# Performance work log

Hardware: AMD Instinct MI355X
Metric: run time of the kernel (lower is better)

The kernel has to match this reference:

```python
import jax, jax.numpy as jnp
import numpy as np

K = 50          # nearest neighbours
IMG = 224       # output mask resolution
SIGMA = 4.0     # gaussian blur sigma -> kernel size 2*round(4*sigma)+1 = 33


def _gaussian_blur(m, sigma=SIGMA):
    # separable gaussian blur with reflect padding (matches cv2 BORDER_REFLECT_101)
    ks = 2 * int(round(4 * sigma)) + 1
    r = ks // 2
    x = jnp.arange(ks, dtype=m.dtype) - r
    k1 = jnp.exp(-(x * x) / (2.0 * sigma * sigma))
    k1 = k1 / jnp.sum(k1)
    p = jnp.pad(m, ((0, 0), (r, r), (r, r), (0, 0)), mode='reflect')
    dn = ('NHWC', 'HWIO', 'NHWC')
    p = jax.lax.conv_general_dilated(p, k1.reshape(ks, 1, 1, 1), (1, 1), 'VALID', dimension_numbers=dn)
    p = jax.lax.conv_general_dilated(p, k1.reshape(1, ks, 1, 1), (1, 1), 'VALID', dimension_numbers=dn)
    return p


def setup_inputs() -> dict:
    key = jax.random.key(0)
    ks = jax.random.split(key, 6)
    B, N = 4, 500
    return {
        'x0': jax.random.normal(ks[0], (B, 28, 28, 512), dtype=jnp.float32),
        'x1': jax.random.normal(ks[1], (B, 14, 14, 1024), dtype=jnp.float32),
        'x2': jax.random.normal(ks[2], (B, 1, 1, 2048), dtype=jnp.float32),
        'f0': jax.random.normal(ks[3], (N, 28, 28, 512), dtype=jnp.float32),
        'f1': jax.random.normal(ks[4], (N, 14, 14, 1024), dtype=jnp.float32),
        'f2': jax.random.normal(ks[5], (N, 1, 1, 2048), dtype=jnp.float32),
    }


def reference(x0, x1, x2, f0, f1, f2):
    B = x2.shape[0]
    N = f2.shape[0]
    q = x2.reshape(B, -1)          # [B, D] pooled query embeddings
    bank = f2.reshape(N, -1)       # [N, D] memory bank embeddings
    # pairwise euclidean distance matrix [B, N]
    d2 = (jnp.sum(q * q, axis=1)[:, None]
          + jnp.sum(bank * bank, axis=1)[None, :]
          - 2.0 * (q @ bank.T))
    dist = jnp.sqrt(jnp.maximum(d2, 0.0))
    # k smallest distances + their indices (== ascending sort truncated at k)
    neg_vals, idx = jax.lax.top_k(-dist, K)   # [B, K]
    score = jnp.mean(-neg_vals, axis=-1, keepdims=True)  # [B, 1]
    masks = []
    for f, x in ((f0, x0), (f1, x1)):
        g = f[idx]                                    # gather: [B, K, H, W, C]
        d = jnp.sqrt(jnp.sum((g - x[:, None]) ** 2, axis=-1))  # [B, K, H, W]
        m = jnp.min(d, axis=1)                        # [B, H, W]
        m = jax.image.resize(m[..., None], (B, IMG, IMG, 1), method='bilinear')
        masks.append(m)
    mask = (masks[0] + masks[1]) / 2.0
    mask = _gaussian_blur(mask)
    return score, mask
```

## Files before the change

### kernel.cpp

```cpp
#include <hip/hip_runtime.h>
#include <math.h>

#define B_ 4
#define N_ 500
#define K_ 50
#define D_ 2048
#define IMG_ 224

__global__ void dist_kernel(const float* __restrict__ x2, const float* __restrict__ f2,
                            float* __restrict__ dist) {
  const int n = blockIdx.x, b = blockIdx.y;
  const float* q = x2 + (size_t)b * D_;
  const float* r = f2 + (size_t)n * D_;
  float s = 0.f;
  for (int c = threadIdx.x; c < D_; c += 256) {
    float d = q[c] - r[c];
    s += d * d;
  }
  for (int o = 32; o; o >>= 1) s += __shfl_down(s, o);
  __shared__ float part[4];
  const int lane = threadIdx.x & 63, wv = threadIdx.x >> 6;
  if (lane == 0) part[wv] = s;
  __syncthreads();
  if (threadIdx.x == 0)
    dist[b * N_ + n] = sqrtf(part[0] + part[1] + part[2] + part[3]);
}

__global__ void topk_kernel(const float* __restrict__ dist, int* __restrict__ idx,
                            float* __restrict__ score) {
  const int b = blockIdx.x;
  const int lane = threadIdx.x;
  float v[8];
  int id[8];
  int cnt = 0;
  for (int n = lane; n < N_; n += 64) { v[cnt] = dist[b * N_ + n]; id[cnt] = n; cnt++; }
  for (int c = cnt; c < 8; c++) { v[c] = INFINITY; id[c] = -1; }
  float ssum = 0.f;
  for (int k = 0; k < K_; k++) {
    float bestv = v[0];
    int besti = 0;
#pragma unroll
    for (int c = 1; c < 8; c++)
      if (v[c] < bestv) { bestv = v[c]; besti = c; }
    unsigned long long key =
        ((unsigned long long)__float_as_uint(bestv) << 32) | (unsigned)lane;
    for (int o = 32; o; o >>= 1) {
      unsigned long long other = __shfl_xor(key, o);
      if (other < key) key = other;
    }
    const int wl = (int)(key & 63u);
    const float wvmin = __uint_as_float((unsigned)(key >> 32));
    if (lane == wl) {
      idx[b * K_ + k] = id[besti];
      v[besti] = INFINITY;
    }
    ssum += wvmin;
  }
  if (lane == 0) score[b] = ssum / (float)K_;
}

template <int C, int H>
__global__ __launch_bounds__(256) void mindist_kernel(
    const float* __restrict__ f, const float* __restrict__ x,
    const int* __restrict__ idx, float* __restrict__ m) {
  const int p = blockIdx.x;
  const int b = p / (H * H);
  const int hw = p % (H * H);
  const int lane = threadIdx.x & 63;
  const int wv = threadIdx.x >> 6;
  constexpr int V = C / 256;
  const float4* xrow = (const float4*)(x + ((size_t)b * H * H + hw) * C);
  float4 xv[V];
#pragma unroll
  for (int i = 0; i < V; i++) xv[i] = xrow[lane + i * 64];
  float best = INFINITY;
  for (int k = wv; k < K_; k += 4) {
    const int n = idx[b * K_ + k];
    const float4* frow = (const float4*)(f + ((size_t)n * H * H + hw) * C);
    float s = 0.f;
#pragma unroll
    for (int i = 0; i < V; i++) {
      float4 fv = frow[lane + i * 64];
      float d0 = fv.x - xv[i].x, d1 = fv.y - xv[i].y;
      float d2 = fv.z - xv[i].z, d3 = fv.w - xv[i].w;
      s += d0 * d0 + d1 * d1 + d2 * d2 + d3 * d3;
    }
    for (int o = 32; o; o >>= 1) s += __shfl_down(s, o);
    if (lane == 0) best = fminf(best, s);
  }
  __shared__ float red[4];
  if (lane == 0) red[wv] = best;
  __syncthreads();
  if (threadIdx.x == 0)
    m[p] = sqrtf(fminf(fminf(red[0], red[1]), fminf(red[2], red[3])));
}

__global__ void gk_kernel(float* __restrict__ gk) {
  __shared__ float w[33];
  const int t = threadIdx.x;
  if (t < 33) {
    float xx = (float)t - 16.f;
    w[t] = expf(-(xx * xx) / 32.f);
  }
  __syncthreads();
  if (t == 0) {
    float s = 0.f;
    for (int i = 0; i < 33; i++) s += w[i];
    for (int i = 0; i < 33; i++) gk[i] = w[i] / s;
  }
}

__device__ inline float bilerp(const float* __restrict__ m, int H, int i, int j) {
  const float scale = (float)H / (float)IMG_;
  float ty = fminf(fmaxf(((float)i + 0.5f) * scale - 0.5f, 0.f), (float)(H - 1));
  float tx = fminf(fmaxf(((float)j + 0.5f) * scale - 0.5f, 0.f), (float)(H - 1));
  const int y0 = (int)ty, x0 = (int)tx;
  const int y1 = y0 + 1 < H ? y0 + 1 : H - 1;
  const int x1 = x0 + 1 < H ? x0 + 1 : H - 1;
  const float wy = ty - (float)y0, wx = tx - (float)x0;
  const float a = m[y0 * H + x0] * (1.f - wx) + m[y0 * H + x1] * wx;
  const float c = m[y1 * H + x0] * (1.f - wx) + m[y1 * H + x1] * wx;
  return a * (1.f - wy) + c * wy;
}

__global__ void upsample_kernel(const float* __restrict__ m0, const float* __restrict__ m1,
                                float* __restrict__ up) {
  const int t = blockIdx.x * 256 + threadIdx.x;
  if (t >= B_ * IMG_ * IMG_) return;
  const int b = t / (IMG_ * IMG_);
  const int r = t % (IMG_ * IMG_);
  const int i = r / IMG_, j = r % IMG_;
  const float a0 = bilerp(m0 + b * 28 * 28, 28, i, j);
  const float a1 = bilerp(m1 + b * 14 * 14, 14, i, j);
  up[t] = 0.5f * (a0 + a1);
}

__device__ inline int reflect101(int t) {
  t = t < 0 ? -t : t;
  t = t > IMG_ - 1 ? 2 * (IMG_ - 1) - t : t;
  return t;
}

__global__ void blurH_kernel(const float* __restrict__ up, float* __restrict__ tmp,
                             const float* __restrict__ gk) {
  const int t = blockIdx.x * 256 + threadIdx.x;
  if (t >= B_ * IMG_ * IMG_) return;
  const int b = t / (IMG_ * IMG_);
  const int r = t % (IMG_ * IMG_);
  const int i = r / IMG_, j = r % IMG_;
  float s = 0.f;
#pragma unroll
  for (int o = 0; o < 33; o++) {
    const int y = reflect101(i - 16 + o);
    s += gk[o] * up[(b * IMG_ + y) * IMG_ + j];
  }
  tmp[t] = s;
}

__global__ void blurW_kernel(const float* __restrict__ tmp, float* __restrict__ outm,
                             const float* __restrict__ gk) {
  const int t = blockIdx.x * 256 + threadIdx.x;
  if (t >= B_ * IMG_ * IMG_) return;
  const int b = t / (IMG_ * IMG_);
  const int r = t % (IMG_ * IMG_);
  const int i = r / IMG_, j = r % IMG_;
  float s = 0.f;
#pragma unroll
  for (int o = 0; o < 33; o++) {
    const int xx = reflect101(j - 16 + o);
    s += gk[o] * tmp[(b * IMG_ + i) * IMG_ + xx];
  }
  outm[t] = s;
}

extern "C" void kernel_launch(void* const* d_in, const int* in_sizes, int n_in,
                              void* d_out, int out_size, void* d_ws, size_t ws_size,
                              hipStream_t stream) {
  const float* x0 = (const float*)d_in[0];
  const float* x1 = (const float*)d_in[1];
  const float* x2 = (const float*)d_in[2];
  const float* f0 = (const float*)d_in[3];
  const float* f1 = (const float*)d_in[4];
  const float* f2 = (const float*)d_in[5];
  float* out = (float*)d_out;

  float* ws = (float*)d_ws;
  float* dist = ws;
  int* idxb = (int*)(ws + 2000);
  float* m0 = ws + 2200;
  float* m1 = ws + 5336;
  float* gk = ws + 6120;
  float* up = ws + 6160;
  float* tmp = ws + 206864;

  dist_kernel<<<dim3(N_, B_), 256, 0, stream>>>(x2, f2, dist);
  topk_kernel<<<B_, 64, 0, stream>>>(dist, idxb, out);
  gk_kernel<<<1, 64, 0, stream>>>(gk);
  mindist_kernel<512, 28><<<B_ * 28 * 28, 256, 0, stream>>>(f0, x0, idxb, m0);
  mindist_kernel<1024, 14><<<B_ * 14 * 14, 256, 0, stream>>>(f1, x1, idxb, m1);
  const int npix = B_ * IMG_ * IMG_;
  upsample_kernel<<<npix / 256, 256, 0, stream>>>(m0, m1, up);
  blurH_kernel<<<npix / 256, 256, 0, stream>>>(up, tmp, gk);
  blurW_kernel<<<npix / 256, 256, 0, stream>>>(tmp, out + B_, gk);
}
```

Baseline: 1.126 ms.

## Fuse mindist launches, prefetch gathered rows, and fuse upsample+blur into tiled kernel

Merges the two per-level min-distance kernels into a single 512-thread launch. That launch caches the top-k indices in shared memory and prefetches the next gathered feature row while the current one is reduced. The upsample, vertical blur and horizontal blur passes become one shared-memory tiled kernel that computes the Gaussian weights in-block, which removes the separate weight kernel and the global intermediates. The reference distance kernel is also vectorised with float4 loads. The costs are more launches and global round-trips avoided, against redundant halo computation per tile and higher register pressure from double-buffered rows.

Measured after the change: 1.117 ms. Within noise of the previous version (-0.8%).

```diff
diff --git a/kernel.cpp b/kernel.cpp
--- a/kernel.cpp
+++ b/kernel.cpp
@@ -10,12 +10,16 @@
 __global__ void dist_kernel(const float* __restrict__ x2, const float* __restrict__ f2,
                             float* __restrict__ dist) {
   const int n = blockIdx.x, b = blockIdx.y;
-  const float* q = x2 + (size_t)b * D_;
-  const float* r = f2 + (size_t)n * D_;
+  const float4* q = (const float4*)(x2 + (size_t)b * D_);
+  const float4* r = (const float4*)(f2 + (size_t)n * D_);
   float s = 0.f;
-  for (int c = threadIdx.x; c < D_; c += 256) {
-    float d = q[c] - r[c];
-    s += d * d;
+#pragma unroll
+  for (int c = 0; c < 2; c++) {
+    const float4 qa = q[threadIdx.x + c * 256];
+    const float4 ra = r[threadIdx.x + c * 256];
+    const float d0 = qa.x - ra.x, d1 = qa.y - ra.y;
+    const float d2 = qa.z - ra.z, d3 = qa.w - ra.w;
+    s += d0 * d0 + d1 * d1 + d2 * d2 + d3 * d3;
   }
   for (int o = 32; o; o >>= 1) s += __shfl_down(s, o);
   __shared__ float part[4];
@@ -60,12 +64,11 @@
 }
 
 template <int C, int H>
-__global__ __launch_bounds__(256) void mindist_kernel(
-    const float* __restrict__ f, const float* __restrict__ x,
-    const int* __restrict__ idx, float* __restrict__ m) {
-  const int p = blockIdx.x;
+__device__ void mindist_body(const float* __restrict__ f, const float* __restrict__ x,
+                             const int* idx_s, float* red, float* __restrict__ m,
+                             const int p) {
   const int b = p / (H * H);
-  const int hw = p % (H * H);
+  const int hw = p - b * (H * H);
   const int lane = threadIdx.x & 63;
   const int wv = threadIdx.x >> 6;
   constexpr int V = C / 256;
@@ -74,40 +77,62 @@
 #pragma unroll
   for (int i = 0; i < V; i++) xv[i] = xrow[lane + i * 64];
   float best = INFINITY;
-  for (int k = wv; k < K_; k += 4) {
-    const int n = idx[b * K_ + k];
-    const float4* frow = (const float4*)(f + ((size_t)n * H * H + hw) * C);
-    float s = 0.f;
-#pragma unroll
-    for (int i = 0; i < V; i++) {
-      float4 fv = frow[lane + i * 64];
-      float d0 = fv.x - xv[i].x, d1 = fv.y - xv[i].y;
-      float d2 = fv.z - xv[i].z, d3 = fv.w - xv[i].w;
-      s += d0 * d0 + d1 * d1 + d2 * d2 + d3 * d3;
+  int k = wv;
+  {
+    const float4* frow = (const float4*)(f + ((size_t)idx_s[k] * H * H + hw) * C);
+    float4 fv[V];
+#pragma unroll
+    for (int i = 0; i < V; i++) fv[i] = frow[lane + i * 64];
+    while (true) {
+      const int k2 = k + 8;
+      float4 gv[V];
+      if (k2 < K_) {
+        const float4* grow = (const float4*)(f + ((size_t)idx_s[k2] * H * H + hw) * C);
+#pragma unroll
+        for (int i = 0; i < V; i++) gv[i] = grow[lane + i * 64];
+      }
+      float s = 0.f;
+#pragma unroll
+      for (int i = 0; i < V; i++) {
+        const float d0 = fv[i].x - xv[i].x, d1 = fv[i].y - xv[i].y;
+        const float d2 = fv[i].z - xv[i].z, d3 = fv[i].w - xv[i].w;
+        s += d0 * d0 + d1 * d1 + d2 * d2 + d3 * d3;
+      }
+#pragma unroll
+      for (int o = 32; o; o >>= 1) s += __shfl_down(s, o);
+      best = fminf(best, s);
+      if (k2 >= K_) break;
+#pragma unroll
+      for (int i = 0; i < V; i++) fv[i] = gv[i];
+      k = k2;
     }
-    for (int o = 32; o; o >>= 1) s += __shfl_down(s, o);
-    if (lane == 0) best = fminf(best, s);
-  }
-  __shared__ float red[4];
+  }
   if (lane == 0) red[wv] = best;
   __syncthreads();
-  if (threadIdx.x == 0)
-    m[p] = sqrtf(fminf(fminf(red[0], red[1]), fminf(red[2], red[3])));
-}
-
-__global__ void gk_kernel(float* __restrict__ gk) {
-  __shared__ float w[33];
-  const int t = threadIdx.x;
-  if (t < 33) {
-    float xx = (float)t - 16.f;
-    w[t] = expf(-(xx * xx) / 32.f);
-  }
-  __syncthreads();
-  if (t == 0) {
-    float s = 0.f;
-    for (int i = 0; i < 33; i++) s += w[i];
-    for (int i = 0; i < 33; i++) gk[i] = w[i] / s;
-  }
+  if (threadIdx.x == 0) {
+    float r = red[0];
+#pragma unroll
+    for (int w = 1; w < 8; w++) r = fminf(r, red[w]);
+    m[p] = sqrtf(r);
+  }
+}
+
+__global__ __launch_bounds__(512) void mindist_all(
+    const float* __restrict__ f0, const float* __restrict__ x0,
+    const float* __restrict__ f1, const float* __restrict__ x1,
+    const int* __restrict__ idx, float* __restrict__ m0, float* __restrict__ m1) {
+  __shared__ int idx_s[K_];
+  __shared__ float red[8];
+  const int bid = blockIdx.x;
+  const int isF1 = bid >= B_ * 28 * 28;
+  const int p = isF1 ? bid - B_ * 28 * 28 : bid;
+  const int b = isF1 ? p / (14 * 14) : p / (28 * 28);
+  if (threadIdx.x < K_) idx_s[threadIdx.x] = idx[b * K_ + threadIdx.x];
+  __syncthreads();
+  if (!isF1)
+    mindist_body<512, 28>(f0, x0, idx_s, red, m0, p);
+  else
+    mindist_body<1024, 14>(f1, x1, idx_s, red, m1, p);
 }
 
 __device__ inline float bilerp(const float* __restrict__ m, int H, int i, int j) {
@@ -123,54 +148,63 @@
   return a * (1.f - wy) + c * wy;
 }
 
-__global__ void upsample_kernel(const float* __restrict__ m0, const float* __restrict__ m1,
-                                float* __restrict__ up) {
-  const int t = blockIdx.x * 256 + threadIdx.x;
-  if (t >= B_ * IMG_ * IMG_) return;
-  const int b = t / (IMG_ * IMG_);
-  const int r = t % (IMG_ * IMG_);
-  const int i = r / IMG_, j = r % IMG_;
-  const float a0 = bilerp(m0 + b * 28 * 28, 28, i, j);
-  const float a1 = bilerp(m1 + b * 14 * 14, 14, i, j);
-  up[t] = 0.5f * (a0 + a1);
-}
-
 __device__ inline int reflect101(int t) {
   t = t < 0 ? -t : t;
   t = t > IMG_ - 1 ? 2 * (IMG_ - 1) - t : t;
   return t;
 }
 
-__global__ void blurH_kernel(const float* __restrict__ up, float* __restrict__ tmp,
-                             const float* __restrict__ gk) {
-  const int t = blockIdx.x * 256 + threadIdx.x;
-  if (t >= B_ * IMG_ * IMG_) return;
-  const int b = t / (IMG_ * IMG_);
-  const int r = t % (IMG_ * IMG_);
-  const int i = r / IMG_, j = r % IMG_;
-  float s = 0.f;
-#pragma unroll
-  for (int o = 0; o < 33; o++) {
-    const int y = reflect101(i - 16 + o);
-    s += gk[o] * up[(b * IMG_ + y) * IMG_ + j];
-  }
-  tmp[t] = s;
-}
-
-__global__ void blurW_kernel(const float* __restrict__ tmp, float* __restrict__ outm,
-                             const float* __restrict__ gk) {
-  const int t = blockIdx.x * 256 + threadIdx.x;
-  if (t >= B_ * IMG_ * IMG_) return;
-  const int b = t / (IMG_ * IMG_);
-  const int r = t % (IMG_ * IMG_);
-  const int i = r / IMG_, j = r % IMG_;
-  float s = 0.f;
-#pragma unroll
-  for (int o = 0; o < 33; o++) {
-    const int xx = reflect101(j - 16 + o);
-    s += gk[o] * tmp[(b * IMG_ + i) * IMG_ + xx];
-  }
-  outm[t] = s;
+__global__ __launch_bounds__(256) void mask_kernel(const float* __restrict__ m0,
+                                                   const float* __restrict__ m1,
+                                                   float* __restrict__ outm) {
+  __shared__ float gk_s[33];
+  __shared__ float inv2;
+  __shared__ float up_s[64][64];
+  __shared__ float tmp_s[32][64];
+  const int tid = threadIdx.x;
+  const int tx0 = blockIdx.x * 32, ty0 = blockIdx.y * 32, b = blockIdx.z;
+
+  if (tid < 33) {
+    const float xx = (float)tid - 16.f;
+    gk_s[tid] = expf(-(xx * xx) / 32.f);
+  }
+  __syncthreads();
+  if (tid == 0) {
+    float s = 0.f;
+#pragma unroll
+    for (int i = 0; i < 33; i++) s += gk_s[i];
+    inv2 = 1.f / (s * s);
+  }
+
+  const float* mb0 = m0 + b * 28 * 28;
+  const float* mb1 = m1 + b * 14 * 14;
+#pragma unroll
+  for (int e = tid; e < 64 * 64; e += 256) {
+    const int yy = e >> 6, xx = e & 63;
+    const int iy = reflect101(ty0 + yy - 16);
+    const int ix = reflect101(tx0 + xx - 16);
+    const float a0 = bilerp(mb0, 28, iy, ix);
+    const float a1 = bilerp(mb1, 14, iy, ix);
+    up_s[yy][xx] = 0.5f * (a0 + a1);
+  }
+  __syncthreads();
+#pragma unroll
+  for (int e = tid; e < 32 * 64; e += 256) {
+    const int y = e >> 6, x = e & 63;
+    float s = 0.f;
+#pragma unroll
+    for (int o = 0; o < 33; o++) s += gk_s[o] * up_s[y + o][x];
+    tmp_s[y][x] = s;
+  }
+  __syncthreads();
+#pragma unroll
+  for (int e = tid; e < 32 * 32; e += 256) {
+    const int y = e >> 5, x = e & 31;
+    float s = 0.f;
+#pragma unroll
+    for (int o = 0; o < 33; o++) s += gk_s[o] * tmp_s[y][x + o];
+    outm[((size_t)b * IMG_ + (ty0 + y)) * IMG_ + (tx0 + x)] = s * inv2;
+  }
 }
 
 extern "C" void kernel_launch(void* const* d_in, const int* in_sizes, int n_in,
@@ -189,17 +223,9 @@
   int* idxb = (int*)(ws + 2000);
   float* m0 = ws + 2200;
   float* m1 = ws + 5336;
-  float* gk = ws + 6120;
-  float* up = ws + 6160;
-  float* tmp = ws + 206864;
 
   dist_kernel<<<dim3(N_, B_), 256, 0, stream>>>(x2, f2, dist);
   topk_kernel<<<B_, 64, 0, stream>>>(dist, idxb, out);
-  gk_kernel<<<1, 64, 0, stream>>>(gk);
-  mindist_kernel<512, 28><<<B_ * 28 * 28, 256, 0, stream>>>(f0, x0, idxb, m0);
-  mindist_kernel<1024, 14><<<B_ * 14 * 14, 256, 0, stream>>>(f1, x1, idxb, m1);
-  const int npix = B_ * IMG_ * IMG_;
-  upsample_kernel<<<npix / 256, 256, 0, stream>>>(m0, m1, up);
-  blurH_kernel<<<npix / 256, 256, 0, stream>>>(up, tmp, gk);
-  blurW_kernel<<<npix / 256, 256, 0, stream>>>(tmp, out + B_, gk);
-}
+  mindist_all<<<B_ * 28 * 28 + B_ * 14 * 14, 512, 0, stream>>>(f0, x0, f1, x1, idxb, m0, m1);
+  mask_kernel<<<dim3(7, 7, B_), 256, 0, stream>>>(m0, m1, out + B_);
+}
```
